# Optimization experiments

Hardware: AMD Instinct MI355X
Metric: run time of the kernel (lower is better)

The kernel has to match this reference:

```python
import jax, jax.numpy as jnp
import numpy as np

CHUNK, STEP, NCHUNK = 75, 25, 22
DIM, HEADS = 64, 8
BN_EPS = 1e-5


def _conv1d(x, w, b):
    # x: [N, Cin, L], w: [Cout, Cin, K] (torch layout), VALID padding, stride 1
    y = jax.lax.conv_general_dilated(x, w, (1,), 'VALID',
                                     dimension_numbers=('NCH', 'OIH', 'NCH'))
    return y + b[None, :, None]


def _bn(x, gamma, beta, mean, var):
    # inference-mode batchnorm over channel dim of [N, C, L]
    scale = gamma / jnp.sqrt(var + BN_EPS)
    return (x - mean[None, :, None]) * scale[None, :, None] + beta[None, :, None]


def _swish(x):
    return x * jax.nn.sigmoid(x)


def _encode(audio, p):
    # audio: [B, 1, L] -> overlapping chunks [B, 22, 1, 75] via gather (unfold)
    B = audio.shape[0]
    idx = np.arange(NCHUNK)[:, None] * STEP + np.arange(CHUNK)[None, :]  # [22, 75]
    x = audio[:, :, idx]                      # [B, 1, 22, 75]
    x = x.transpose(0, 2, 1, 3).reshape(B * NCHUNK, 1, CHUNK)
    x = _swish(_bn(_conv1d(x, p['w1'], p['b1']), p['g1'], p['be1'], p['m1'], p['v1']))  # [B*22,16,50]
    x = _swish(_bn(_conv1d(x, p['w2'], p['b2']), p['g2'], p['be2'], p['m2'], p['v2']))  # [B*22,32,25]
    x = _swish(_bn(_conv1d(x, p['w3'], p['b3']), p['g3'], p['be3'], p['m3'], p['v3']))  # [B*22,64,1]
    return x[:, :, 0].reshape(B, NCHUNK, DIM)  # concat over chunks == seq of 22 tokens


def _mha(feat, p):
    # per-head full-width linears (torch Linear: y = x @ W.T + b), stacked over heads
    # Wq/Wk/Wv: [H, D, D]; bq/bk/bv: [H, D]
    B, S, D = feat.shape
    Q = jnp.einsum('bsd,hed->bhse', feat, p['Wq']) + p['bq'][None, :, None, :]
    K = jnp.einsum('bsd,hed->bhse', feat, p['Wk']) + p['bk'][None, :, None, :]
    V = jnp.einsum('bsd,hed->bhse', feat, p['Wv']) + p['bv'][None, :, None, :]
    A = jax.nn.softmax(jnp.einsum('bhse,bhte->bhst', Q, K), axis=-1)  # no 1/sqrt(d) scaling in source
    O = jnp.einsum('bhst,bhte->bhse', A, V)       # [B, H, S, D]
    O = O.transpose(0, 2, 1, 3).reshape(B, S, HEADS * D)  # concat heads along feature dim
    return O @ p['Wfc'].T + p['bfc']              # [B, S, D]


def setup_inputs() -> dict:
    key = jax.random.key(0)
    ks = jax.random.split(key, 16)
    B, L = 4096, 600
    C1, C2 = DIM // 4, DIM // 2
    inp = {
        'audio_vec1': jax.random.normal(ks[0], (B, 1, L), jnp.float32),
        'audio_vec2': jax.random.normal(ks[1], (B, 1, L), jnp.float32),
        # conv stack
        'w1': jax.random.normal(ks[2], (C1, 1, 26), jnp.float32) * 0.05,
        'b1': jnp.zeros((C1,), jnp.float32),
        'g1': jnp.ones((C1,), jnp.float32), 'be1': jnp.zeros((C1,), jnp.float32),
        'm1': jnp.zeros((C1,), jnp.float32), 'v1': jnp.ones((C1,), jnp.float32),
        'w2': jax.random.normal(ks[3], (C2, C1, 26), jnp.float32) * 0.05,
        'b2': jnp.zeros((C2,), jnp.float32),
        'g2': jnp.ones((C2,), jnp.float32), 'be2': jnp.zeros((C2,), jnp.float32),
        'm2': jnp.zeros((C2,), jnp.float32), 'v2': jnp.ones((C2,), jnp.float32),
        'w3': jax.random.normal(ks[4], (DIM, C2, 25), jnp.float32) * 0.05,
        'b3': jnp.zeros((DIM,), jnp.float32),
        'g3': jnp.ones((DIM,), jnp.float32), 'be3': jnp.zeros((DIM,), jnp.float32),
        'm3': jnp.zeros((DIM,), jnp.float32), 'v3': jnp.ones((DIM,), jnp.float32),
        # attention (per-head full-width projections)
        'Wq': jax.random.normal(ks[5], (HEADS, DIM, DIM), jnp.float32) * 0.05,
        'bq': jnp.zeros((HEADS, DIM), jnp.float32),
        'Wk': jax.random.normal(ks[6], (HEADS, DIM, DIM), jnp.float32) * 0.05,
        'bk': jnp.zeros((HEADS, DIM), jnp.float32),
        'Wv': jax.random.normal(ks[7], (HEADS, DIM, DIM), jnp.float32) * 0.05,
        'bv': jnp.zeros((HEADS, DIM), jnp.float32),
        'Wfc': jax.random.normal(ks[8], (DIM, HEADS * DIM), jnp.float32) * 0.05,
        'bfc': jnp.zeros((DIM,), jnp.float32),
        # final fc
        'Wout': jax.random.normal(ks[9], (DIM, DIM), jnp.float32) * 0.05,
        'bout': jnp.zeros((DIM,), jnp.float32),
    }
    return inp


def reference(audio_vec1, audio_vec2, w1, b1, g1, be1, m1, v1,
              w2, b2, g2, be2, m2, v2, w3, b3, g3, be3, m3, v3,
              Wq, bq, Wk, bk, Wv, bv, Wfc, bfc, Wout, bout):
    p = dict(w1=w1, b1=b1, g1=g1, be1=be1, m1=m1, v1=v1,
             w2=w2, b2=b2, g2=g2, be2=be2, m2=m2, v2=v2,
             w3=w3, b3=b3, g3=g3, be3=be3, m3=m3, v3=v3,
             Wq=Wq, bq=bq, Wk=Wk, bk=bk, Wv=Wv, bv=bv, Wfc=Wfc, bfc=bfc)
    f1 = _encode(audio_vec1, p)   # [B, 22, 64]
    f2 = _encode(audio_vec2, p)
    f1 = _mha(f1, p).mean(axis=1) @ Wout.T + bout  # [B, 64]
    f2 = _mha(f2, p).mean(axis=1) @ Wout.T + bout
    return (f1, f2)
```

## Files before the change

### kernel.cpp

```cpp
#include <hip/hip_runtime.h>
#include <hip/hip_bf16.h>
#include <math.h>

#define NCHUNK 22
#define SEQLEN 600
#define BN_EPS 1e-5f

#define OFF_W1F    0
#define OFF_W2F    1024
#define OFF_W3F    14336
#define OFF_MHF    65536
#define OFF_WC     98304
#define OFF_UH     131072
#define OFF_WH     131584
#define OFF_CH     132096
#define OFF_CBIAS  132104
#define OFF_WCOMB  132168
#define OFF_FEAT   164936
#define REPACK_N   132104

typedef short bf16x8 __attribute__((ext_vector_type(8)));
typedef float f32x4 __attribute__((ext_vector_type(4)));
typedef float f32x16 __attribute__((ext_vector_type(16)));

#if __has_builtin(__builtin_amdgcn_perm)
#define PERM_HI(r0, r1) __builtin_amdgcn_perm((r1), (r0), 0x05040100u)
#define PERM_LO(r0, r1) __builtin_amdgcn_perm((r1), (r0), 0x07060302u)
#else
#define PERM_HI(r0, r1) (((r0) & 0xFFFFu) | ((r1) << 16))
#define PERM_LO(r0, r1) (((r0) >> 16) | ((r1) & 0xFFFF0000u))
#endif

__device__ __forceinline__ float swishf(float z) {
    return z / (1.f + __expf(-z));
}
__device__ __forceinline__ unsigned short bf16_rne(float f) {
    __hip_bfloat16 h = __float2bfloat16(f);
    unsigned short u; __builtin_memcpy(&u, &h, 2); return u;
}
__device__ __forceinline__ float bf16_tof(unsigned short h) {
    return __uint_as_float(((unsigned int)h) << 16);
}
__device__ __forceinline__ unsigned int pk2(float f0, float f1) {
    __hip_bfloat162 b2;
    b2.x = __float2bfloat16(f0);
    b2.y = __float2bfloat16(f1);
    unsigned int r; __builtin_memcpy(&r, &b2, 4); return r;
}
__device__ __forceinline__ unsigned int pack_hl(float f) {
    unsigned short h = bf16_rne(f);
    unsigned short l = bf16_rne(f - bf16_tof(h));
    return (unsigned int)h | ((unsigned int)l << 16);
}
__device__ __forceinline__ float unpk_f32(unsigned int w) {
    return __uint_as_float(w << 16) + __uint_as_float(w & 0xFFFF0000u);
}
__device__ __forceinline__ unsigned int dup_word(float f, int pat) {
    unsigned short h = bf16_rne(f);
    unsigned short v = pat ? bf16_rne(f - bf16_tof(h)) : h;
    return (unsigned int)v | ((unsigned int)v << 16);
}
__device__ __forceinline__ unsigned int frag_word(float f0, float f1, int hl) {
    unsigned short h0 = bf16_rne(f0), h1 = bf16_rne(f1);
    if (hl == 0) return (unsigned int)h0 | ((unsigned int)h1 << 16);
    unsigned short l0 = bf16_rne(f0 - bf16_tof(h0));
    unsigned short l1 = bf16_rne(f1 - bf16_tof(h1));
    return (unsigned int)l0 | ((unsigned int)l1 << 16);
}
__device__ __forceinline__ void frag_from_packed(const unsigned int* p, bf16x8& h8, bf16x8& l8) {
    unsigned int r0 = p[0], r1 = p[1], r2 = p[2], r3 = p[3];
    unsigned int r4 = p[4], r5 = p[5], r6 = p[6], r7 = p[7];
    union U { unsigned int w[4]; bf16x8 v; } H, L;
    H.w[0] = PERM_HI(r0, r1); H.w[1] = PERM_HI(r2, r3);
    H.w[2] = PERM_HI(r4, r5); H.w[3] = PERM_HI(r6, r7);
    L.w[0] = PERM_LO(r0, r1); L.w[1] = PERM_LO(r2, r3);
    L.w[2] = PERM_LO(r4, r5); L.w[3] = PERM_LO(r6, r7);
    h8 = H.v; l8 = L.v;
}

__global__ __launch_bounds__(256) void repack_kernel(
    const float* __restrict__ w1, const float* __restrict__ w2, const float* __restrict__ w3,
    const float* __restrict__ Wq, const float* __restrict__ Wk, const float* __restrict__ Wv,
    const float* __restrict__ Wfc, const float* __restrict__ Wout,
    const float* __restrict__ bq, const float* __restrict__ bk,
    float* __restrict__ ws)
{
    int tid = blockIdx.x * 256 + threadIdx.x;
    unsigned int* wsu = (unsigned int*)ws;
    if (tid < 1024) {
        int r = tid & 3, lane = (tid >> 2) & 63, pat = (tid >> 8) & 1, ph = (tid >> 9) & 1;
        int li = lane & 15, lg = lane >> 4;
        int k = ph * 16 + lg * 4 + r;
        float f = (k < 26) ? w1[li * 26 + k] : 0.f;
        wsu[OFF_W1F + tid] = dup_word(f, pat);
    }
    int t2 = tid - 1024;
    if (t2 >= 0 && t2 < 13312) {
        int r = t2 & 3, lane = (t2 >> 2) & 63, hl = (t2 >> 8) & 1, s = t2 >> 9;
        int co = lane & 31;
        int ci0 = (lane >> 5) * 8;
        float f0 = w2[co * 416 + (ci0 + 2 * r) * 26 + s];
        float f1 = w2[co * 416 + (ci0 + 2 * r + 1) * 26 + s];
        wsu[OFF_W2F + t2] = frag_word(f0, f1, hl);
    }
    int t3 = tid - 14336;
    if (t3 >= 0 && t3 < 51200) {
        int r = t3 & 3, l = (t3 >> 2) & 63, hl = (t3 >> 8) & 1;
        int nt = (t3 >> 9) & 3, s = t3 >> 11;
        int co = nt * 16 + (l & 15);
        int k0 = s * 32 + (l >> 4) * 8 + 2 * r;
        float f0 = w3[co * 800 + (k0 & 31) * 25 + (k0 >> 5)];
        float f1 = w3[co * 800 + ((k0 + 1) & 31) * 25 + ((k0 + 1) >> 5)];
        wsu[OFF_W3F + t3] = frag_word(f0, f1, hl);
    }
    int t4 = tid - 65536;
    if (t4 >= 0 && t4 < 32768) {
        int r = t4 & 3, l = (t4 >> 2) & 63, hl = (t4 >> 8) & 1;
        int nt = (t4 >> 9) & 3, ks = (t4 >> 11) & 1, h = t4 >> 12;
        int n = nt * 16 + (l & 15);
        int d0 = ks * 32 + (l >> 4) * 8 + 2 * r;
        const float* wqh = Wq + h * 4096;
        const float* wkh = Wk + h * 4096;
        float f0 = 0.f, f1 = 0.f;
        #pragma unroll 8
        for (int e = 0; e < 64; ++e) {
            float wk_en = wkh[e * 64 + n];
            f0 = fmaf(wqh[e * 64 + d0],     wk_en, f0);
            f1 = fmaf(wqh[e * 64 + d0 + 1], wk_en, f1);
        }
        wsu[OFF_MHF + t4] = frag_word(f0, f1, hl);
    }
    int t7 = tid - 98304;
    if (t7 >= 0 && t7 < 32768) {
        int k = t7 & 63, j = t7 >> 6;
        float acc = 0.f;
        #pragma unroll 8
        for (int d = 0; d < 64; ++d)
            acc = fmaf(Wfc[d * 512 + j], Wout[k * 64 + d], acc);
        ws[OFF_WCOMB + t7] = acc;
    }
    int t8 = tid - 131072;
    if (t8 >= 0 && t8 < 512) {
        int h = t8 >> 6, d = t8 & 63;
        float acc = 0.f;
        #pragma unroll 8
        for (int e = 0; e < 64; ++e) acc = fmaf(Wq[h * 4096 + e * 64 + d], bk[h * 64 + e], acc);
        ws[OFF_UH + t8] = acc;
    }
    int t9 = tid - 131584;
    if (t9 >= 0 && t9 < 512) {
        int h = t9 >> 6, d = t9 & 63;
        float acc = 0.f;
        #pragma unroll 8
        for (int e = 0; e < 64; ++e) acc = fmaf(Wk[h * 4096 + e * 64 + d], bq[h * 64 + e], acc);
        ws[OFF_WH + t9] = acc;
    }
    int t10 = tid - 132096;
    if (t10 >= 0 && t10 < 8) {
        float acc = 0.f;
        #pragma unroll 8
        for (int e = 0; e < 64; ++e) acc = fmaf(bq[t10 * 64 + e], bk[t10 * 64 + e], acc);
        ws[OFF_CH + t10] = acc;
    }
}

__global__ __launch_bounds__(256) void repack2_kernel(
    const float* __restrict__ Wv, float* __restrict__ ws)
{
    int tid = blockIdx.x * 256 + threadIdx.x;
    int k = tid & 63, j = tid >> 6;
    int h = j >> 6, d = j & 63;
    const float* wcomb = ws + OFF_WCOMB + (size_t)(h * 64) * 64 + k;
    const float* wv = Wv + h * 4096 + d;
    float acc = 0.f;
    #pragma unroll 8
    for (int e = 0; e < 64; ++e)
        acc = fmaf(wv[e * 64], wcomb[e * 64], acc);
    ws[OFF_WC + tid] = acc;
}

__global__ __launch_bounds__(64) void cbias_kernel(
    const float* __restrict__ Wfc, const float* __restrict__ Wout,
    const float* __restrict__ bfc, const float* __restrict__ bout,
    const float* __restrict__ bv, float* __restrict__ ws)
{
    __shared__ float sd_s[64];
    int t = threadIdx.x;
    float acc = 0.f;
    for (int j = 0; j < 512; ++j) acc = fmaf(bv[j], Wfc[t * 512 + j], acc);
    sd_s[t] = acc;
    __syncthreads();
    float cb = bout[t];
    #pragma unroll 8
    for (int dp = 0; dp < 64; ++dp) cb = fmaf(bfc[dp] + sd_s[dp], Wout[t * 64 + dp], cb);
    ws[OFF_CBIAS + t] = cb;
}

__global__ __launch_bounds__(256, 4) void encoder_kernel(
    const float* __restrict__ audio1, const float* __restrict__ audio2,
    const float* __restrict__ b1, const float* __restrict__ g1, const float* __restrict__ be1,
    const float* __restrict__ m1, const float* __restrict__ v1,
    const float* __restrict__ b2, const float* __restrict__ g2, const float* __restrict__ be2,
    const float* __restrict__ m2, const float* __restrict__ v2,
    const float* __restrict__ b3, const float* __restrict__ g3, const float* __restrict__ be3,
    const float* __restrict__ m3, const float* __restrict__ v3,
    float* __restrict__ ws, int B)
{
    __shared__ __align__(16) unsigned int smem[8816];
    unsigned int* a_p0 = smem;
    unsigned int* a_p1 = smem + 192;
    unsigned int* w2f  = smem + 384;
    unsigned short* y1h0 = (unsigned short*)(smem + 2432);
    unsigned short* y1l0 = (unsigned short*)(smem + 3972);
    unsigned short* y1h1 = (unsigned short*)(smem + 5512);
    unsigned short* y1l1 = (unsigned short*)(smem + 7052);
    unsigned short* y2h0 = (unsigned short*)(smem + 384);
    unsigned short* y2l0 = (unsigned short*)(smem + 2404);
    unsigned short* y2h1 = (unsigned short*)(smem + 4424);
    unsigned short* y2l1 = (unsigned short*)(smem + 6444);
    float* A_s  = (float*)(smem + 8592);
    float* Bc_s = (float*)(smem + 8704);

    int t = threadIdx.x;
    int blk = blockIdx.x;
    int g0 = blk * 2, g1v = g0 + 1;
    int seq0 = g0 / 5, tile0 = g0 - seq0 * 5;
    int seq1 = g1v / 5, tile1 = g1v - seq1 * 5;
    int tc0 = (tile0 == 4) ? 2 : 5, tc1 = (tile1 == 4) ? 2 : 5;
    int nq0 = 25 * tc0, nq1 = 25 * tc1;
    int ny10 = nq0 + 25, ny11 = nq1 + 25;
    int na0 = nq0 + 50, na1 = nq1 + 50;
    const unsigned int* wsu = (const unsigned int*)ws;
    int lane = t & 63, wid = t >> 6;
    int li = lane & 15, lg = lane >> 4;

    const float* aud0 = (seq0 < B ? audio1 + (size_t)seq0 * SEQLEN
                                  : audio2 + (size_t)(seq0 - B) * SEQLEN) + tile0 * 125;
    const float* aud1 = (seq1 < B ? audio1 + (size_t)seq1 * SEQLEN
                                  : audio2 + (size_t)(seq1 - B) * SEQLEN) + tile1 * 125;
    uint4 w1b[2][2];
    #pragma unroll
    for (int ph = 0; ph < 2; ++ph)
        #pragma unroll
        for (int pat = 0; pat < 2; ++pat)
            w1b[ph][pat] = *(const uint4*)(wsu + OFF_W1F + ((ph * 2 + pat) * 64 + lane) * 4);

    if (t < 192) {
        a_p0[t] = (t < na0) ? pack_hl(aud0[t]) : 0u;
        a_p1[t] = (t < na1) ? pack_hl(aud1[t]) : 0u;
    }
    *(uint4*)(w2f + t * 4) = *(const uint4*)(wsu + OFF_W2F + t * 4);
    if (t < 16)       { float A = g1[t] * rsqrtf(v1[t] + BN_EPS); A_s[t] = A; Bc_s[t] = (b1[t] - m1[t]) * A + be1[t]; }
    else if (t < 48)  { int i = t - 16; float A = g2[i] * rsqrtf(v2[i] + BN_EPS); A_s[t] = A; Bc_s[t] = (b2[i] - m2[i]) * A + be2[i]; }
    else if (t < 112) { int i = t - 48; float A = g3[i] * rsqrtf(v3[i] + BN_EPS); A_s[t] = A; Bc_s[t] = (b3[i] - m3[i]) * A + be3[i]; }
    for (int i = ny10 * 10 + t; i < 1540; i += 256) {
        (smem + 2432)[i] = 0u;
        (smem + 3972)[i] = 0u;
    }
    for (int i = ny11 * 10 + t; i < 1540; i += 256) {
        (smem + 5512)[i] = 0u;
        (smem + 7052)[i] = 0u;
    }
    __syncthreads();

    {
        float Ai = A_s[li], Bi = Bc_s[li];
        #pragma unroll
        for (int tl = 0; tl < 2; ++tl) {
            const unsigned int* ap_base = tl ? a_p1 : a_p0;
            unsigned short* yh = tl ? y1h1 : y1h0;
            unsigned short* yl = tl ? y1l1 : y1l0;
            int ny1 = tl ? ny11 : ny10;
            int nMt1 = (ny1 + 15) >> 4;
            for (int mt = wid; mt < nMt1; mt += 4) {
                f32x4 acc = {0.f, 0.f, 0.f, 0.f};
                #pragma unroll
                for (int ph = 0; ph < 2; ++ph) {
                    const unsigned int* ap = ap_base + mt * 16 + li + ph * 16 + lg * 4;
                    union { unsigned int w[4]; bf16x8 v; } A;
                    A.w[0] = ap[0]; A.w[1] = ap[1]; A.w[2] = ap[2]; A.w[3] = ap[3];
                    bf16x8 b0 = *(const bf16x8*)&w1b[ph][0];
                    bf16x8 b1 = *(const bf16x8*)&w1b[ph][1];
                    acc = __builtin_amdgcn_mfma_f32_16x16x32_bf16(A.v, b0, acc, 0, 0, 0);
                    acc = __builtin_amdgcn_mfma_f32_16x16x32_bf16(A.v, b1, acc, 0, 0, 0);
                }
                int p0 = mt * 16 + lg * 4;
                #pragma unroll
                for (int rg = 0; rg < 4; rg += 2) {
                    float f0 = swishf(fmaf(acc[rg],     Ai, Bi));
                    float f1 = swishf(fmaf(acc[rg + 1], Ai, Bi));
                    unsigned int hp = pk2(f0, f1);
                    unsigned int lp = pk2(f0 - bf16_tof((unsigned short)hp),
                                          f1 - bf16_tof((unsigned short)(hp >> 16)));
                    int p = p0 + rg;
                    if (p < ny1) {
                        yh[p * 20 + li] = (unsigned short)hp;
                        yl[p * 20 + li] = (unsigned short)lp;
                    }
                    if (p + 1 < ny1) {
                        yh[(p + 1) * 20 + li] = (unsigned short)(hp >> 16);
                        yl[(p + 1) * 20 + li] = (unsigned short)(lp >> 16);
                    }
                }
            }
        }
    }
    __syncthreads();

    int row0 = wid * 32 + (lane & 31);
    int ci0 = (lane >> 5) * 8;
    f32x16 accA, accB;
    #pragma unroll
    for (int r = 0; r < 16; ++r) { accA[r] = 0.f; accB[r] = 0.f; }

    for (int stg = 0; stg < 13; ++stg) {
        uint4 vnext;
        if (stg < 12)
            vnext = *(const uint4*)(wsu + OFF_W2F + (stg + 1) * 1024 + t * 4);
        const unsigned int* cur = w2f + (stg & 1) * 1024;
        #pragma unroll
        for (int half = 0; half < 2; ++half) {
            int s = stg * 2 + half;
            bf16x8 bh = *(const bf16x8*)(cur + half * 512 + lane * 4);
            bf16x8 bl = *(const bf16x8*)(cur + half * 512 + 256 + lane * 4);
            {
                const unsigned short* hp = y1h0 + (row0 + s) * 20 + ci0;
                const unsigned short* lp = y1l0 + (row0 + s) * 20 + ci0;
                union { uint2 u[2]; bf16x8 v; } Ah, Al;
                Ah.u[0] = *(const uint2*)hp; Ah.u[1] = *(const uint2*)(hp + 4);
                Al.u[0] = *(const uint2*)lp; Al.u[1] = *(const uint2*)(lp + 4);
                accA = __builtin_amdgcn_mfma_f32_32x32x16_bf16(Ah.v, bh, accA, 0, 0, 0);
                accA = __builtin_amdgcn_mfma_f32_32x32x16_bf16(Al.v, bh, accA, 0, 0, 0);
                accA = __builtin_amdgcn_mfma_f32_32x32x16_bf16(Ah.v, bl, accA, 0, 0, 0);
            }
            {
                const unsigned short* hp = y1h1 + (row0 + s) * 20 + ci0;
                const unsigned short* lp = y1l1 + (row0 + s) * 20 + ci0;
                union { uint2 u[2]; bf16x8 v; } Ah, Al;
                Ah.u[0] = *(const uint2*)hp; Ah.u[1] = *(const uint2*)(hp + 4);
                Al.u[0] = *(const uint2*)lp; Al.u[1] = *(const uint2*)(lp + 4);
                accB = __builtin_amdgcn_mfma_f32_32x32x16_bf16(Ah.v, bh, accB, 0, 0, 0);
                accB = __builtin_amdgcn_mfma_f32_32x32x16_bf16(Al.v, bh, accB, 0, 0, 0);
                accB = __builtin_amdgcn_mfma_f32_32x32x16_bf16(Ah.v, bl, accB, 0, 0, 0);
            }
        }
        if (stg < 12)
            *(uint4*)(w2f + ((stg + 1) & 1) * 1024 + t * 4) = vnext;
        __syncthreads();
    }
    {
        int co = lane & 31;
        float Ac = A_s[16 + co], Bc = Bc_s[16 + co];
        int rbase = 4 * (lane >> 5) + wid * 32;
        #pragma unroll
        for (int rg = 0; rg < 16; rg += 2) {
            int q0 = rbase + (rg & 3) + 8 * (rg >> 2);
            {
                float f0 = swishf(fmaf(accA[rg],     Ac, Bc));
                float f1 = swishf(fmaf(accA[rg + 1], Ac, Bc));
                unsigned int hp = pk2(f0, f1);
                unsigned int lp = pk2(f0 - bf16_tof((unsigned short)hp),
                                      f1 - bf16_tof((unsigned short)(hp >> 16)));
                if (q0 < nq0) {
                    int cc = q0 / 25, qp = q0 - cc * 25;
                    y2h0[cc * 808 + qp * 32 + co] = (unsigned short)hp;
                    y2l0[cc * 808 + qp * 32 + co] = (unsigned short)lp;
                }
                if (q0 + 1 < nq0) {
                    int cc = (q0 + 1) / 25, qp = (q0 + 1) - cc * 25;
                    y2h0[cc * 808 + qp * 32 + co] = (unsigned short)(hp >> 16);
                    y2l0[cc * 808 + qp * 32 + co] = (unsigned short)(lp >> 16);
                }
            }
            {
                float f0 = swishf(fmaf(accB[rg],     Ac, Bc));
                float f1 = swishf(fmaf(accB[rg + 1], Ac, Bc));
                unsigned int hp = pk2(f0, f1);
                unsigned int lp = pk2(f0 - bf16_tof((unsigned short)hp),
                                      f1 - bf16_tof((unsigned short)(hp >> 16)));
                if (q0 < nq1) {
                    int cc = q0 / 25, qp = q0 - cc * 25;
                    y2h1[cc * 808 + qp * 32 + co] = (unsigned short)hp;
                    y2l1[cc * 808 + qp * 32 + co] = (unsigned short)lp;
                }
                if (q0 + 1 < nq1) {
                    int cc = (q0 + 1) / 25, qp = (q0 + 1) - cc * 25;
                    y2h1[cc * 808 + qp * 32 + co] = (unsigned short)(hp >> 16);
                    y2l1[cc * 808 + qp * 32 + co] = (unsigned short)(lp >> 16);
                }
            }
        }
    }
    __syncthreads();

    {
        const uint4* w3f4 = (const uint4*)(wsu + OFF_W3F);
        f32x4 acc3 = {0.f, 0.f, 0.f, 0.f};
        for (int b5 = 0; b5 < 5; ++b5) {
            uint4 BH[5], BL[5];
            #pragma unroll
            for (int i = 0; i < 5; ++i) {
                int s = b5 * 5 + i;
                BH[i] = w3f4[((s * 4 + wid) * 2 + 0) * 64 + lane];
                BL[i] = w3f4[((s * 4 + wid) * 2 + 1) * 64 + lane];
            }
            #pragma unroll
            for (int i = 0; i < 5; ++i) {
                int s = b5 * 5 + i;
                bf16x8 ah = {}, al = {};
                if (li < 5) {
                    if (li < tc0) {
                        ah = *(const bf16x8*)(y2h0 + li * 808 + s * 32 + lg * 8);
                        al = *(const bf16x8*)(y2l0 + li * 808 + s * 32 + lg * 8);
                    }
                } else if (li < 10) {
                    int c = li - 5;
                    if (c < tc1) {
                        ah = *(const bf16x8*)(y2h1 + c * 808 + s * 32 + lg * 8);
                        al = *(const bf16x8*)(y2l1 + c * 808 + s * 32 + lg * 8);
                    }
                }
                bf16x8 bh = *(const bf16x8*)&BH[i];
                bf16x8 bl = *(const bf16x8*)&BL[i];
                acc3 = __builtin_amdgcn_mfma_f32_16x16x32_bf16(ah, bh, acc3, 0, 0, 0);
                acc3 = __builtin_amdgcn_mfma_f32_16x16x32_bf16(al, bh, acc3, 0, 0, 0);
                acc3 = __builtin_amdgcn_mfma_f32_16x16x32_bf16(ah, bl, acc3, 0, 0, 0);
            }
        }
        int co = wid * 16 + li;
        float A3 = A_s[48 + co], B3 = Bc_s[48 + co];
        unsigned int* featp = (unsigned int*)ws + OFF_FEAT;
        #pragma unroll
        for (int rg = 0; rg < 4; rg += 2) {
            float f0 = swishf(fmaf(acc3[rg],     A3, B3));
            float f1 = swishf(fmaf(acc3[rg + 1], A3, B3));
            unsigned int hp = pk2(f0, f1);
            unsigned int lp = pk2(f0 - bf16_tof((unsigned short)hp),
                                  f1 - bf16_tof((unsigned short)(hp >> 16)));
            unsigned int val0 = (hp & 0xFFFFu) | (lp << 16);
            unsigned int val1 = (hp >> 16) | (lp & 0xFFFF0000u);
            int cc0 = lg * 4 + rg;
            #pragma unroll
            for (int d = 0; d < 2; ++d) {
                int cc = cc0 + d;
                unsigned int val = d ? val1 : val0;
                if (cc < 5) {
                    if (cc < tc0)
                        featp[((size_t)(seq0 * NCHUNK + tile0 * 5 + cc)) * 64 + co] = val;
                } else if (cc < 10) {
                    int c = cc - 5;
                    if (c < tc1)
                        featp[((size_t)(seq1 * NCHUNK + tile1 * 5 + c)) * 64 + co] = val;
                }
            }
        }
    }
}

__global__ __launch_bounds__(256, 4) void mha_kernel(
    const float* __restrict__ ws, float* __restrict__ out, int B)
{
    __shared__ __align__(16) unsigned int smem[9928];
    unsigned int* f_p = smem;
    float* fbar_s = (float*)(smem + 9416);
    float* fred   = (float*)smem;

    int t = threadIdx.x, b = blockIdx.x;
    int lane = t & 63, wid = t >> 6;
    int li = lane & 15, lg = lane >> 4;
    const unsigned int* wsu = (const unsigned int*)ws;
    const unsigned int* featp = wsu + OFF_FEAT + (size_t)b * 1408;
    for (int i = t; i < 1408; i += 256)
        f_p[(i >> 6) * 68 + (i & 63)] = featp[i];
    __syncthreads();

    unsigned short* qh_w = (unsigned short*)(smem + 1496 + wid * 1496);
    unsigned short* ql_w = qh_w + 1496;
    float* P = (float*)(smem + 7480) + wid * 484;

    float rowqv;
    {
        int hl = lane / 22; if (hl > 1) hl = 1;
        int s = lane - hl * 22; if (s > 21) s = 21;
        int h = wid * 2 + hl;
        float acc = ws[OFF_CH + h];
        const float* uh = ws + OFF_UH + h * 64;
        #pragma unroll 8
        for (int d = 0; d < 64; ++d)
            acc = fmaf(unpk_f32(f_p[s * 68 + d]), uh[d], acc);
        rowqv = acc;
    }

    bf16x8 fah[2][2], fal[2][2];
    #pragma unroll
    for (int mt = 0; mt < 2; ++mt)
        #pragma unroll
        for (int ks = 0; ks < 2; ++ks)
            frag_from_packed(f_p + (mt * 16 + li) * 68 + ks * 32 + lg * 8,
                             fah[mt][ks], fal[mt][ks]);

    const uint4* mhf4 = (const uint4*)(wsu + OFF_MHF);

    #pragma unroll
    for (int hh = 0; hh < 2; ++hh) {
        int h = wid * 2 + hh;
        f32x4 a0t0 = {0,0,0,0}, a0t1 = a0t0, a0t2 = a0t0, a0t3 = a0t0;
        f32x4 a1t0 = a0t0, a1t1 = a0t0, a1t2 = a0t0, a1t3 = a0t0;
        #pragma unroll
        for (int nt = 0; nt < 4; ++nt) {
            f32x4 r0 = {0,0,0,0}, r1 = {0,0,0,0};
            #pragma unroll
            for (int ks = 0; ks < 2; ++ks) {
                uint4 bh4 = mhf4[h * 1024 + ks * 512 + nt * 128 + lane];
                uint4 bl4 = mhf4[h * 1024 + ks * 512 + nt * 128 + 64 + lane];
                bf16x8 bh = *(const bf16x8*)&bh4;
                bf16x8 bl = *(const bf16x8*)&bl4;
                r0 = __builtin_amdgcn_mfma_f32_16x16x32_bf16(fah[0][ks], bh, r0, 0, 0, 0);
                r0 = __builtin_amdgcn_mfma_f32_16x16x32_bf16(fal[0][ks], bh, r0, 0, 0, 0);
                r0 = __builtin_amdgcn_mfma_f32_16x16x32_bf16(fah[0][ks], bl, r0, 0, 0, 0);
                r1 = __builtin_amdgcn_mfma_f32_16x16x32_bf16(fah[1][ks], bh, r1, 0, 0, 0);
                r1 = __builtin_amdgcn_mfma_f32_16x16x32_bf16(fal[1][ks], bh, r1, 0, 0, 0);
                r1 = __builtin_amdgcn_mfma_f32_16x16x32_bf16(fah[1][ks], bl, r1, 0, 0, 0);
            }
            if (nt == 0) { a0t0 = r0; a1t0 = r1; }
            else if (nt == 1) { a0t1 = r0; a1t1 = r1; }
            else if (nt == 2) { a0t2 = r0; a1t2 = r1; }
            else { a0t3 = r0; a1t3 = r1; }
        }
        #pragma unroll
        for (int nt = 0; nt < 4; ++nt) {
            int col = nt * 16 + li;
            float wv = ws[OFF_WH + h * 64 + col];
            f32x4 r0 = (nt == 0) ? a0t0 : (nt == 1) ? a0t1 : (nt == 2) ? a0t2 : a0t3;
            f32x4 r1 = (nt == 0) ? a1t0 : (nt == 1) ? a1t1 : (nt == 2) ? a1t2 : a1t3;
            #pragma unroll
            for (int rg = 0; rg < 4; rg += 2) {
                int rowA = lg * 4 + rg;
                {
                    float v0 = r0[rg] + wv, v1 = r0[rg + 1] + wv;
                    unsigned int hp = pk2(v0, v1);
                    unsigned int lp = pk2(v0 - bf16_tof((unsigned short)hp),
                                          v1 - bf16_tof((unsigned short)(hp >> 16)));
                    qh_w[rowA * 68 + col] = (unsigned short)hp;
                    ql_w[rowA * 68 + col] = (unsigned short)lp;
                    qh_w[(rowA + 1) * 68 + col] = (unsigned short)(hp >> 16);
                    ql_w[(rowA + 1) * 68 + col] = (unsigned short)(lp >> 16);
                }
                int rowB = 16 + rowA;
                if (rowB < 22) {
                    float v0 = r1[rg] + wv, v1 = r1[rg + 1] + wv;
                    unsigned int hp = pk2(v0, v1);
                    unsigned int lp = pk2(v0 - bf16_tof((unsigned short)hp),
                                          v1 - bf16_tof((unsigned short)(hp >> 16)));
                    qh_w[rowB * 68 + col] = (unsigned short)hp;
                    ql_w[rowB * 68 + col] = (unsigned short)lp;
                    if (rowB + 1 < 22) {
                        qh_w[(rowB + 1) * 68 + col] = (unsigned short)(hp >> 16);
                        ql_w[(rowB + 1) * 68 + col] = (unsigned short)(lp >> 16);
                    }
                }
            }
        }
        #pragma unroll
        for (int mt = 0; mt < 2; ++mt) {
            union { uint2 u[2]; bf16x8 v; } Th0, Tl0, Th1, Tl1;
            {
                const unsigned short* hp = qh_w + (mt * 16 + li) * 68 + lg * 8;
                const unsigned short* lp = ql_w + (mt * 16 + li) * 68 + lg * 8;
                Th0.u[0] = *(const uint2*)hp;        Th0.u[1] = *(const uint2*)(hp + 4);
                Tl0.u[0] = *(const uint2*)lp;        Tl0.u[1] = *(const uint2*)(lp + 4);
                Th1.u[0] = *(const uint2*)(hp + 32); Th1.u[1] = *(const uint2*)(hp + 36);
                Tl1.u[0] = *(const uint2*)(lp + 32); Tl1.u[1] = *(const uint2*)(lp + 36);
            }
            #pragma unroll
            for (int ntile = 0; ntile < 2; ++ntile) {
                f32x4 sacc = {0, 0, 0, 0};
                sacc = __builtin_amdgcn_mfma_f32_16x16x32_bf16(Th0.v, fah[ntile][0], sacc, 0, 0, 0);
                sacc = __builtin_amdgcn_mfma_f32_16x16x32_bf16(Tl0.v, fah[ntile][0], sacc, 0, 0, 0);
                sacc = __builtin_amdgcn_mfma_f32_16x16x32_bf16(Th0.v, fal[ntile][0], sacc, 0, 0, 0);
                sacc = __builtin_amdgcn_mfma_f32_16x16x32_bf16(Th1.v, fah[ntile][1], sacc, 0, 0, 0);
                sacc = __builtin_amdgcn_mfma_f32_16x16x32_bf16(Tl1.v, fah[ntile][1], sacc, 0, 0, 0);
                sacc = __builtin_amdgcn_mfma_f32_16x16x32_bf16(Th1.v, fal[ntile][1], sacc, 0, 0, 0);
                int u = ntile * 16 + li;
                #pragma unroll
                for (int r = 0; r < 4; ++r) {
                    int s = mt * 16 + lg * 4 + r;
                    float rq = __shfl(rowqv, hh * 22 + (s < 22 ? s : 0));
                    if (s < 22 && u < 22)
                        P[s * 22 + u] = sacc[r] + rq;
                }
            }
        }
        {
            int r2 = lane >> 1, c2 = lane & 1;
            float pm = -1e30f, psum = 0.f;
            if (lane < 44) {
                #pragma unroll
                for (int j = 0; j < 11; ++j) pm = fmaxf(pm, P[r2 * 22 + c2 * 11 + j]);
            }
            float m = fmaxf(__shfl(pm, 2 * lane), __shfl(pm, 2 * lane + 1));
            float rm = __shfl(m, r2);
            if (lane < 44) {
                #pragma unroll
                for (int j = 0; j < 11; ++j) {
                    int idx = r2 * 22 + c2 * 11 + j;
                    float ev = __expf(P[idx] - rm);
                    P[idx] = ev;
                    psum += ev;
                }
            }
            float sum = __shfl(psum, 2 * lane) + __shfl(psum, 2 * lane + 1);
            float rinv = 1.f / sum;
            float a = 0.f;
            #pragma unroll
            for (int s = 0; s < 22; ++s) {
                float rv = __shfl(rinv, s);
                if (lane < 22) a = fmaf(P[s * 22 + lane], rv, a);
            }
            float av = a * (1.f / 22.f);
            float acc = 0.f;
            #pragma unroll
            for (int u = 0; u < 22; ++u) {
                float au = __shfl(av, u);
                acc = fmaf(au, unpk_f32(f_p[u * 68 + lane]), acc);
            }
            fbar_s[h * 64 + lane] = acc;
        }
    }
    __syncthreads();
    {
        int d = t & 63, part = t >> 6;
        const float* wc = ws + OFF_WC;
        float acc = 0.f;
        for (int j = part * 128; j < part * 128 + 128; ++j)
            acc = fmaf(fbar_s[j], wc[j * 64 + d], acc);
        fred[part * 64 + d] = acc;
    }
    __syncthreads();
    if (t < 64)
        out[(size_t)b * 64 + t] = ws[OFF_CBIAS + t]
            + fred[t] + fred[64 + t] + fred[128 + t] + fred[192 + t];
}

extern "C" void kernel_launch(void* const* d_in, const int* in_sizes, int n_in,
                              void* d_out, int out_size, void* d_ws, size_t ws_size,
                              hipStream_t stream) {
    const float* audio1 = (const float*)d_in[0];
    const float* audio2 = (const float*)d_in[1];
    const float* w1   = (const float*)d_in[2];
    const float* b1   = (const float*)d_in[3];
    const float* g1   = (const float*)d_in[4];
    const float* be1  = (const float*)d_in[5];
    const float* m1   = (const float*)d_in[6];
    const float* v1   = (const float*)d_in[7];
    const float* w2   = (const float*)d_in[8];
    const float* b2   = (const float*)d_in[9];
    const float* g2   = (const float*)d_in[10];
    const float* be2  = (const float*)d_in[11];
    const float* m2   = (const float*)d_in[12];
    const float* v2   = (const float*)d_in[13];
    const float* w3   = (const float*)d_in[14];
    const float* b3   = (const float*)d_in[15];
    const float* g3   = (const float*)d_in[16];
    const float* be3  = (const float*)d_in[17];
    const float* m3   = (const float*)d_in[18];
    const float* v3   = (const float*)d_in[19];
    const float* Wq   = (const float*)d_in[20];
    const float* bq   = (const float*)d_in[21];
    const float* Wk   = (const float*)d_in[22];
    const float* bk   = (const float*)d_in[23];
    const float* Wv   = (const float*)d_in[24];
    const float* bv   = (const float*)d_in[25];
    const float* Wfc  = (const float*)d_in[26];
    const float* bfc  = (const float*)d_in[27];
    const float* Wout = (const float*)d_in[28];
    const float* bout = (const float*)d_in[29];

    float* ws  = (float*)d_ws;
    float* out = (float*)d_out;
    int B = in_sizes[0] / SEQLEN;
    int nseq = 2 * B;
    int npair = nseq * 5 / 2;

    repack_kernel<<<(REPACK_N + 255) / 256, 256, 0, stream>>>(
        w1, w2, w3, Wq, Wk, Wv, Wfc, Wout, bq, bk, ws);
    repack2_kernel<<<128, 256, 0, stream>>>(Wv, ws);
    cbias_kernel<<<1, 64, 0, stream>>>(Wfc, Wout, bfc, bout, bv, ws);
    encoder_kernel<<<npair, 256, 0, stream>>>(audio1, audio2,
        b1, g1, be1, m1, v1,
        b2, g2, be2, m2, v2,
        b3, g3, be3, m3, v3,
        ws, B);
    mha_kernel<<<nseq, 256, 0, stream>>>(ws, out, B);
}
```

Measured before the change: 755.9 us.

## Process three audio tiles per encoder block instead of two

Each encoder block now handles three 5-chunk tiles instead of two, so each staged conv2 weight slice feeds three MFMA accumulator sets. This amortizes the weight loads to shared memory, the BN parameter setup and the per-block overhead over more work. In exchange it uses more shared memory and registers (a third f32x16 accumulator), lowers the occupancy hint from 4 to 3 blocks, and adds bounds guards for a partial last block. The conv3 stage now packs up to 15 chunks into the 16-row MFMA tile, using more of rows that were previously left idle.

```diff
diff --git a/kernel.cpp b/kernel.cpp
--- a/kernel.cpp
+++ b/kernel.cpp
@@ -196,7 +196,7 @@
     ws[OFF_CBIAS + t] = cb;
 }
 
-__global__ __launch_bounds__(256, 4) void encoder_kernel(
+__global__ __launch_bounds__(256, 3) void encoder_kernel(
     const float* __restrict__ audio1, const float* __restrict__ audio2,
     const float* __restrict__ b1, const float* __restrict__ g1, const float* __restrict__ be1,
     const float* __restrict__ m1, const float* __restrict__ v1,
@@ -206,30 +206,41 @@
     const float* __restrict__ m3, const float* __restrict__ v3,
     float* __restrict__ ws, int B)
 {
-    __shared__ __align__(16) unsigned int smem[8816];
-    unsigned int* a_p0 = smem;
-    unsigned int* a_p1 = smem + 192;
-    unsigned int* w2f  = smem + 384;
-    unsigned short* y1h0 = (unsigned short*)(smem + 2432);
-    unsigned short* y1l0 = (unsigned short*)(smem + 3972);
-    unsigned short* y1h1 = (unsigned short*)(smem + 5512);
-    unsigned short* y1l1 = (unsigned short*)(smem + 7052);
-    unsigned short* y2h0 = (unsigned short*)(smem + 384);
-    unsigned short* y2l0 = (unsigned short*)(smem + 2404);
-    unsigned short* y2h1 = (unsigned short*)(smem + 4424);
-    unsigned short* y2l1 = (unsigned short*)(smem + 6444);
-    float* A_s  = (float*)(smem + 8592);
-    float* Bc_s = (float*)(smem + 8704);
+    __shared__ __align__(16) unsigned int smem[12344];
+    float* A_s  = (float*)smem;
+    float* Bc_s = (float*)(smem + 112);
+    unsigned int* a_p0 = smem + 224;
+    unsigned int* a_p1 = smem + 416;
+    unsigned int* a_p2 = smem + 608;
+    unsigned int* w2f  = smem + 800;
+    unsigned short* y1h0 = (unsigned short*)(smem + 2848);
+    unsigned short* y1l0 = (unsigned short*)(smem + 4388);
+    unsigned short* y1h1 = (unsigned short*)(smem + 5928);
+    unsigned short* y1l1 = (unsigned short*)(smem + 7468);
+    unsigned short* y1h2 = (unsigned short*)(smem + 9008);
+    unsigned short* y1l2 = (unsigned short*)(smem + 10548);
+    unsigned short* y2h0 = (unsigned short*)(smem + 224);
+    unsigned short* y2l0 = (unsigned short*)(smem + 2244);
+    unsigned short* y2h1 = (unsigned short*)(smem + 4264);
+    unsigned short* y2l1 = (unsigned short*)(smem + 6284);
+    unsigned short* y2h2 = (unsigned short*)(smem + 8304);
+    unsigned short* y2l2 = (unsigned short*)(smem + 10324);
 
     int t = threadIdx.x;
     int blk = blockIdx.x;
-    int g0 = blk * 2, g1v = g0 + 1;
-    int seq0 = g0 / 5, tile0 = g0 - seq0 * 5;
-    int seq1 = g1v / 5, tile1 = g1v - seq1 * 5;
-    int tc0 = (tile0 == 4) ? 2 : 5, tc1 = (tile1 == 4) ? 2 : 5;
-    int nq0 = 25 * tc0, nq1 = 25 * tc1;
-    int ny10 = nq0 + 25, ny11 = nq1 + 25;
-    int na0 = nq0 + 50, na1 = nq1 + 50;
+    int ntile = 10 * B;
+    int g0 = blk * 3, g1v = g0 + 1, g2v = g0 + 2;
+    bool v1ok = g1v < ntile, v2ok = g2v < ntile;
+    int gc1 = v1ok ? g1v : 0, gc2 = v2ok ? g2v : 0;
+    int seq0 = g0 / 5,  tile0 = g0 - seq0 * 5;
+    int seq1 = gc1 / 5, tile1 = gc1 - seq1 * 5;
+    int seq2 = gc2 / 5, tile2 = gc2 - seq2 * 5;
+    int tc0 = (tile0 == 4) ? 2 : 5;
+    int tc1 = v1ok ? ((tile1 == 4) ? 2 : 5) : 0;
+    int tc2 = v2ok ? ((tile2 == 4) ? 2 : 5) : 0;
+    int nq0 = 25 * tc0, nq1 = 25 * tc1, nq2 = 25 * tc2;
+    int ny10 = nq0 + 25, ny11 = nq1 + 25, ny12 = nq2 + 25;
+    int na0 = nq0 + 50, na1 = nq1 + 50, na2 = nq2 + 50;
     const unsigned int* wsu = (const unsigned int*)ws;
     int lane = t & 63, wid = t >> 6;
     int li = lane & 15, lg = lane >> 4;
@@ -238,6 +249,8 @@
                                   : audio2 + (size_t)(seq0 - B) * SEQLEN) + tile0 * 125;
     const float* aud1 = (seq1 < B ? audio1 + (size_t)seq1 * SEQLEN
                                   : audio2 + (size_t)(seq1 - B) * SEQLEN) + tile1 * 125;
+    const float* aud2 = (seq2 < B ? audio1 + (size_t)seq2 * SEQLEN
+                                  : audio2 + (size_t)(seq2 - B) * SEQLEN) + tile2 * 125;
     uint4 w1b[2][2];
     #pragma unroll
     for (int ph = 0; ph < 2; ++ph)
@@ -248,29 +261,31 @@
     if (t < 192) {
         a_p0[t] = (t < na0) ? pack_hl(aud0[t]) : 0u;
         a_p1[t] = (t < na1) ? pack_hl(aud1[t]) : 0u;
+        a_p2[t] = (t < na2) ? pack_hl(aud2[t]) : 0u;
     }
     *(uint4*)(w2f + t * 4) = *(const uint4*)(wsu + OFF_W2F + t * 4);
     if (t < 16)       { float A = g1[t] * rsqrtf(v1[t] + BN_EPS); A_s[t] = A; Bc_s[t] = (b1[t] - m1[t]) * A + be1[t]; }
     else if (t < 48)  { int i = t - 16; float A = g2[i] * rsqrtf(v2[i] + BN_EPS); A_s[t] = A; Bc_s[t] = (b2[i] - m2[i]) * A + be2[i]; }
     else if (t < 112) { int i = t - 48; float A = g3[i] * rsqrtf(v3[i] + BN_EPS); A_s[t] = A; Bc_s[t] = (b3[i] - m3[i]) * A + be3[i]; }
     for (int i = ny10 * 10 + t; i < 1540; i += 256) {
-        (smem + 2432)[i] = 0u;
-        (smem + 3972)[i] = 0u;
+        (smem + 2848)[i] = 0u; (smem + 4388)[i] = 0u;
     }
     for (int i = ny11 * 10 + t; i < 1540; i += 256) {
-        (smem + 5512)[i] = 0u;
-        (smem + 7052)[i] = 0u;
+        (smem + 5928)[i] = 0u; (smem + 7468)[i] = 0u;
+    }
+    for (int i = ny12 * 10 + t; i < 1540; i += 256) {
+        (smem + 9008)[i] = 0u; (smem + 10548)[i] = 0u;
     }
     __syncthreads();
 
     {
         float Ai = A_s[li], Bi = Bc_s[li];
         #pragma unroll
-        for (int tl = 0; tl < 2; ++tl) {
-            const unsigned int* ap_base = tl ? a_p1 : a_p0;
-            unsigned short* yh = tl ? y1h1 : y1h0;
-            unsigned short* yl = tl ? y1l1 : y1l0;
-            int ny1 = tl ? ny11 : ny10;
+        for (int tl = 0; tl < 3; ++tl) {
+            const unsigned int* ap_base = (tl == 0) ? a_p0 : (tl == 1) ? a_p1 : a_p2;
+            unsigned short* yh = (tl == 0) ? y1h0 : (tl == 1) ? y1h1 : y1h2;
+            unsigned short* yl = (tl == 0) ? y1l0 : (tl == 1) ? y1l1 : y1l2;
+            int ny1 = (tl == 0) ? ny10 : (tl == 1) ? ny11 : ny12;
             int nMt1 = (ny1 + 15) >> 4;
             for (int mt = wid; mt < nMt1; mt += 4) {
                 f32x4 acc = {0.f, 0.f, 0.f, 0.f};
@@ -309,9 +324,9 @@
 
     int row0 = wid * 32 + (lane & 31);
     int ci0 = (lane >> 5) * 8;
-    f32x16 accA, accB;
+    f32x16 accA, accB, accC;
     #pragma unroll
-    for (int r = 0; r < 16; ++r) { accA[r] = 0.f; accB[r] = 0.f; }
+    for (int r = 0; r < 16; ++r) { accA[r] = 0.f; accB[r] = 0.f; accC[r] = 0.f; }
 
     for (int stg = 0; stg < 13; ++stg) {
         uint4 vnext;
@@ -343,6 +358,16 @@
                 accB = __builtin_amdgcn_mfma_f32_32x32x16_bf16(Al.v, bh, accB, 0, 0, 0);
                 accB = __builtin_amdgcn_mfma_f32_32x32x16_bf16(Ah.v, bl, accB, 0, 0, 0);
             }
+            {
+                const unsigned short* hp = y1h2 + (row0 + s) * 20 + ci0;
+                const unsigned short* lp = y1l2 + (row0 + s) * 20 + ci0;
+                union { uint2 u[2]; bf16x8 v; } Ah, Al;
+                Ah.u[0] = *(const uint2*)hp; Ah.u[1] = *(const uint2*)(hp + 4);
+                Al.u[0] = *(const uint2*)lp; Al.u[1] = *(const uint2*)(lp + 4);
+                accC = __builtin_amdgcn_mfma_f32_32x32x16_bf16(Ah.v, bh, accC, 0, 0, 0);
+                accC = __builtin_amdgcn_mfma_f32_32x32x16_bf16(Al.v, bh, accC, 0, 0, 0);
+                accC = __builtin_amdgcn_mfma_f32_32x32x16_bf16(Ah.v, bl, accC, 0, 0, 0);
+            }
         }
         if (stg < 12)
             *(uint4*)(w2f + ((stg + 1) & 1) * 1024 + t * 4) = vnext;
@@ -387,6 +412,23 @@
                     int cc = (q0 + 1) / 25, qp = (q0 + 1) - cc * 25;
                     y2h1[cc * 808 + qp * 32 + co] = (unsigned short)(hp >> 16);
                     y2l1[cc * 808 + qp * 32 + co] = (unsigned short)(lp >> 16);
+                }
+            }
+            {
+                float f0 = swishf(fmaf(accC[rg],     Ac, Bc));
+                float f1 = swishf(fmaf(accC[rg + 1], Ac, Bc));
+                unsigned int hp = pk2(f0, f1);
+                unsigned int lp = pk2(f0 - bf16_tof((unsigned short)hp),
+                                      f1 - bf16_tof((unsigned short)(hp >> 16)));
+                if (q0 < nq2) {
+                    int cc = q0 / 25, qp = q0 - cc * 25;
+                    y2h2[cc * 808 + qp * 32 + co] = (unsigned short)hp;
+                    y2l2[cc * 808 + qp * 32 + co] = (unsigned short)lp;
+                }
+                if (q0 + 1 < nq2) {
+                    int cc = (q0 + 1) / 25, qp = (q0 + 1) - cc * 25;
+                    y2h2[cc * 808 + qp * 32 + co] = (unsigned short)(hp >> 16);
+                    y2l2[cc * 808 + qp * 32 + co] = (unsigned short)(lp >> 16);
                 }
             }
         }
@@ -418,6 +460,12 @@
                     if (c < tc1) {
                         ah = *(const bf16x8*)(y2h1 + c * 808 + s * 32 + lg * 8);
                         al = *(const bf16x8*)(y2l1 + c * 808 + s * 32 + lg * 8);
+                    }
+                } else if (li < 15) {
+                    int c = li - 10;
+                    if (c < tc2) {
+                        ah = *(const bf16x8*)(y2h2 + c * 808 + s * 32 + lg * 8);
+                        al = *(const bf16x8*)(y2l2 + c * 808 + s * 32 + lg * 8);
                     }
                 }
                 bf16x8 bh = *(const bf16x8*)&BH[i];
@@ -451,6 +499,10 @@
                     int c = cc - 5;
                     if (c < tc1)
                         featp[((size_t)(seq1 * NCHUNK + tile1 * 5 + c)) * 64 + co] = val;
+                } else if (cc < 15) {
+                    int c = cc - 10;
+                    if (c < tc2)
+                        featp[((size_t)(seq2 * NCHUNK + tile2 * 5 + c)) * 64 + co] = val;
                 }
             }
         }
@@ -680,13 +732,13 @@
     float* out = (float*)d_out;
     int B = in_sizes[0] / SEQLEN;
     int nseq = 2 * B;
-    int npair = nseq * 5 / 2;
+    int ntri = (nseq * 5 + 2) / 3;
 
     repack_kernel<<<(REPACK_N + 255) / 256, 256, 0, stream>>>(
         w1, w2, w3, Wq, Wk, Wv, Wfc, Wout, bq, bk, ws);
     repack2_kernel<<<128, 256, 0, stream>>>(Wv, ws);
     cbias_kernel<<<1, 64, 0, stream>>>(Wfc, Wout, bfc, bout, bv, ws);
-    encoder_kernel<<<npair, 256, 0, stream>>>(audio1, audio2,
+    encoder_kernel<<<ntri, 256, 0, stream>>>(audio1, audio2,
         b1, g1, be1, m1, v1,
         b2, g2, be2, m2, v2,
         b3, g3, be3, m3, v3,
```

Measured after the change: 725.9 us. 4.0% less time.
